# Kernel tuning notes

Hardware: AMD Instinct MI355X
Metric: run time of the kernel (lower is better)

The kernel has to match this reference:

```python
import jax, jax.numpy as jnp
import numpy as np
from jax import lax

E = 1024      # embed_dim
H = 16        # num_heads
HD = E // H   # head_dim = 64
GS = 2        # head_group_size
G = H // GS   # num head groups = 8
KQ = 3        # kq kernel q size
KK = 3        # kq kernel k size


def setup_inputs() -> dict:
    key = jax.random.key(0)
    ks = jax.random.split(key, 18)
    B, S = 2, 1024
    def rn(k, shape, scale=1.0):
        return jax.random.normal(k, shape, dtype=jnp.float32) * scale
    return {
        "Q": rn(ks[0], (B, S, E)),
        "K": rn(ks[1], (B, S, E)),
        "V": rn(ks[2], (B, S, E)),
        "Wq": rn(ks[3], (E, E), 0.02), "bq": rn(ks[4], (E,), 0.02),
        "Wk": rn(ks[5], (E, E), 0.02), "bk": rn(ks[6], (E,), 0.02),
        "Wv": rn(ks[7], (E, E), 0.02), "bv": rn(ks[8], (E,), 0.02),
        "Wo": rn(ks[9], (E, E), 0.02), "bo": rn(ks[10], (E,), 0.02),
        # depthwise key-query conv: [out=H, in/groups=1, KQ, KK]
        "kq_w": rn(ks[11], (H, 1, KQ, KK), 0.1),
        "kq_b": rn(ks[12], (H,), 0.02),
        # grouped 1x1 head-mix conv: weight [H, GS] (kernel dim squeezed), bias [H]
        "mix_w": rn(ks[13], (H, GS), 0.3),
        "mix_b": rn(ks[14], (H,), 0.02),
        # DynamicTanh params over head_dim (channels_last)
        "dyt_alpha": jnp.array([0.5], dtype=jnp.float32),
        "dyt_w": jnp.ones((HD,), dtype=jnp.float32),
        "dyt_b": jnp.zeros((HD,), dtype=jnp.float32),
        "depth_scale": jnp.ones((1,), dtype=jnp.float32),
    }


def reference(Q, K, V, Wq, bq, Wk, bk, Wv, bv, Wo, bo,
              kq_w, kq_b, mix_w, mix_b, dyt_alpha, dyt_w, dyt_b, depth_scale):
    B, S, _ = Q.shape
    scale = HD ** (-0.5)
    # projections -> [B, H, S, HD]
    q = (Q @ Wq + bq).reshape(B, S, H, HD).transpose(0, 2, 1, 3)
    k = (K @ Wk + bk).reshape(B, S, H, HD).transpose(0, 2, 1, 3)
    v = (V @ Wv + bv).reshape(B, S, H, HD).transpose(0, 2, 1, 3)

    # raw logits [B, H, Sq, Sk], multiplicative causal mask (zeros above diag)
    logits = jnp.einsum('bhqd,bhkd->bhqk', q, k) * scale
    causal = jnp.tril(jnp.ones((S, S), dtype=logits.dtype))
    logits = logits * causal

    # per-head (depthwise) key-query conv2d; torch pads q-dim by 2 both sides
    # then crops to first S rows (causal in q), k-dim padded symmetrically by 1
    conv = lax.conv_general_dilated(
        logits, kq_w, window_strides=(1, 1),
        padding=[(KQ - 1, KQ - 1), ((KK - 1) // 2, (KK - 1) // 2)],
        dimension_numbers=('NCHW', 'OIHW', 'NCHW'),
        feature_group_count=H)
    conv = conv + kq_b[None, :, None, None]
    conv = conv[:, :, :S, :]

    attn = jax.nn.softmax(conv, axis=-1)

    # grouped 1x1 head-mixing conv (within groups of GS heads) + bias
    attn_g = attn.reshape(B, G, GS, S, S)
    mw = mix_w.reshape(G, GS, GS)  # [group, out_in_group, in_in_group]
    mixed = jnp.einsum('goj,bgjqk->bgoqk', mw, attn_g).reshape(B, H, S, S)
    mixed = mixed + mix_b[None, :, None, None]

    out = jnp.einsum('bhqk,bhkd->bhqd', mixed, v)
    # DynamicTanh over head_dim (channels_last) + depth scale
    out = jnp.tanh(dyt_alpha * out) * dyt_w + dyt_b
    out = out * depth_scale
    out = out.transpose(0, 2, 1, 3).reshape(B, S, E)
    return out @ Wo + bo
```

## Files before the change

### kernel.cpp

```cpp
#include <hip/hip_runtime.h>
#include <cstdint>
#include <cstddef>

typedef __bf16 bf16;
typedef __bf16 bf16x8 __attribute__((ext_vector_type(8)));
typedef float f32x4 __attribute__((ext_vector_type(4)));

#define DEVI static __device__ __forceinline__

DEVI unsigned int cvt_pk_bf16(float lo, float hi) {
  unsigned int bl = __float_as_uint(lo);
  bl += 0x7fffu + ((bl >> 16) & 1u);
  unsigned int bh = __float_as_uint(hi);
  bh += 0x7fffu + ((bh >> 16) & 1u);
  return (bl >> 16) | (bh & 0xffff0000u);
}
DEVI float bf_lo(unsigned int u) { return __uint_as_float(u << 16); }
DEVI float bf_hi(unsigned int u) { return __uint_as_float(u & 0xffff0000u); }

DEVI void gload16(const bf16* g, bf16* l) {
  __builtin_amdgcn_global_load_lds(
      (const __attribute__((address_space(1))) unsigned int*)g,
      (__attribute__((address_space(3))) unsigned int*)l, 16, 0, 0);
}

__global__ __launch_bounds__(256) void prep_k(
    const float* __restrict__ Wq, const float* __restrict__ Wk,
    const float* __restrict__ Wv, const float* __restrict__ Wo,
    const float* __restrict__ Q, const float* __restrict__ K,
    const float* __restrict__ V, bf16* __restrict__ Wt,
    bf16* __restrict__ Ab)
{
  __shared__ bf16 Ts[64 * 72];
  const int bid = blockIdx.x, tid = threadIdx.x;
  if (bid < 1024) {
    const int z = bid >> 8;
    const float* W = (z == 0) ? Wq : (z == 1) ? Wk : (z == 2) ? Wv : Wo;
    bf16* out = Wt + ((size_t)z << 20);
    const int n0 = (bid & 15) * 64, k0 = ((bid >> 4) & 15) * 64;
    #pragma unroll
    for (int i = 0; i < 4; ++i) {
      int t = tid + i * 256;
      int kr = t >> 4, nc = t & 15;
      float4 v = *(const float4*)(W + (size_t)(k0 + kr) * 1024 + n0 + nc * 4);
      Ts[(nc * 4 + 0) * 72 + kr] = (bf16)v.x;
      Ts[(nc * 4 + 1) * 72 + kr] = (bf16)v.y;
      Ts[(nc * 4 + 2) * 72 + kr] = (bf16)v.z;
      Ts[(nc * 4 + 3) * 72 + kr] = (bf16)v.w;
    }
    __syncthreads();
    const int n = tid >> 2, kc = tid & 3;
    *(uint4*)(out + (size_t)(n0 + n) * 1024 + k0 + kc * 16) =
        *(const uint4*)(&Ts[n * 72 + kc * 16]);
    *(uint4*)(out + (size_t)(n0 + n) * 1024 + k0 + kc * 16 + 8) =
        *(const uint4*)(&Ts[n * 72 + kc * 16 + 8]);
  } else {
    const int t = bid - 1024;
    const int z = t >> 10, x = t & 1023;
    const float* A = (z == 0) ? Q : (z == 1) ? K : V;
    bf16* o = Ab + ((size_t)z << 21);
    const size_t idx = (size_t)x * 256 + tid;
    const float4 v0 = *(const float4*)(A + idx * 8);
    const float4 v1 = *(const float4*)(A + idx * 8 + 4);
    uint4 u;
    u.x = cvt_pk_bf16(v0.x, v0.y);
    u.y = cvt_pk_bf16(v0.z, v0.w);
    u.z = cvt_pk_bf16(v1.x, v1.y);
    u.w = cvt_pk_bf16(v1.z, v1.w);
    *(uint4*)(o + idx * 8) = u;
  }
}

__global__ __launch_bounds__(256) void proj_gemm_k(
    const bf16* __restrict__ Ab, const bf16* __restrict__ Wt,
    const float* __restrict__ bq, const float* __restrict__ bk,
    const float* __restrict__ bv, bf16* __restrict__ outbase,
    float* __restrict__ Tsum)
{
  const int z = blockIdx.z;
  const bf16* A  = Ab + ((size_t)z << 21);
  const bf16* Bt = Wt + ((size_t)z << 20);
  const float* bias = (z == 0) ? bq : (z == 1) ? bk : bv;
  bf16* outb = outbase + ((size_t)z << 21);

  __shared__ __align__(16) bf16 Asm[2][8192];
  __shared__ __align__(16) bf16 Bsm[2][4096];

  const int tid = threadIdx.x, lane = tid & 63, wid = tid >> 6;
  const int q4 = lane >> 4, n16 = lane & 15;
  const int wm = wid >> 1, wn = wid & 1;
  const int bid = blockIdx.x;
  const int m0 = (bid & 15) * 128, n0 = (bid >> 4) * 64;

  const int cbase = wid * 64 + lane;
  const bf16* gA[4];
  #pragma unroll
  for (int i = 0; i < 4; ++i) {
    int cc = cbase + i * 256;
    gA[i] = A + (size_t)(m0 + (cc >> 3)) * 1024 + (((cc & 7) ^ ((cc >> 3) & 7)) << 3);
  }
  const bf16* gB[2];
  #pragma unroll
  for (int i = 0; i < 2; ++i) {
    int cc = cbase + i * 256;
    gB[i] = Bt + (size_t)(n0 + (cc >> 3)) * 1024 + (((cc & 7) ^ ((cc >> 3) & 7)) << 3);
  }
  const int swl = n16 & 7;

  f32x4 acc[4][2] = {};

  #pragma unroll
  for (int i = 0; i < 4; ++i) gload16(gA[i], &Asm[0][i * 2048 + wid * 512]);
  #pragma unroll
  for (int i = 0; i < 2; ++i) gload16(gB[i], &Bsm[0][i * 2048 + wid * 512]);
  __syncthreads();

  int cur = 0;
  for (int t = 0; t < 16; ++t) {
    if (t < 15) {
      const int kc = (t + 1) * 64;
      #pragma unroll
      for (int i = 0; i < 4; ++i) gload16(gA[i] + kc, &Asm[cur ^ 1][i * 2048 + wid * 512]);
      #pragma unroll
      for (int i = 0; i < 2; ++i) gload16(gB[i] + kc, &Bsm[cur ^ 1][i * 2048 + wid * 512]);
    }
    const char* ab = (const char*)&Asm[cur][0];
    const char* bb = (const char*)&Bsm[cur][0];
    bf16x8 af[2][4], bfv[2][2];
    #pragma unroll
    for (int kk2 = 0; kk2 < 2; ++kk2) {
      #pragma unroll
      for (int rt = 0; rt < 4; ++rt)
        af[kk2][rt] = *(const bf16x8*)(ab + (wm * 64 + rt * 16 + n16) * 128 +
                                       (((kk2 * 4 + q4) ^ swl) << 4));
      #pragma unroll
      for (int ct = 0; ct < 2; ++ct)
        bfv[kk2][ct] = *(const bf16x8*)(bb + (wn * 32 + ct * 16 + n16) * 128 +
                                        (((kk2 * 4 + q4) ^ swl) << 4));
    }
    #pragma unroll
    for (int kk2 = 0; kk2 < 2; ++kk2)
      #pragma unroll
      for (int rt = 0; rt < 4; ++rt)
        #pragma unroll
        for (int ct = 0; ct < 2; ++ct)
          acc[rt][ct] = __builtin_amdgcn_mfma_f32_16x16x32_bf16(af[kk2][rt], bfv[kk2][ct], acc[rt][ct], 0, 0, 0);
    __syncthreads();
    cur ^= 1;
  }

  if (z < 2) {
    const int h = n0 >> 6;
    #pragma unroll
    for (int ct = 0; ct < 2; ++ct) {
      const int dl = wn * 32 + ct * 16 + n16;
      const float bvl = bias[n0 + dl];
      #pragma unroll
      for (int rt = 0; rt < 4; ++rt) {
        #pragma unroll
        for (int r = 0; r < 4; ++r) {
          int row = m0 + wm * 64 + rt * 16 + q4 * 4 + r;
          int b2 = row >> 10, s = row & 1023;
          outb[((size_t)((b2 * 16 + h) * 1024 + s) << 6) + dl] =
              (bf16)(acc[rt][ct][r] + bvl);
        }
      }
    }
  } else {
    const int b2 = m0 >> 10, kt0 = (m0 & 1023) >> 6, hh = n0 >> 6;
    bf16* vout = outb + ((size_t)(b2 * 16 + hh) << 16) + (size_t)(kt0 + wm) * 4096;
    float csum[2] = {0.f, 0.f};
    #pragma unroll
    for (int rt = 0; rt < 4; ++rt) {
      const int kk = rt >> 1;
      const int q4c = (rt & 1) * 2 + (q4 >> 1);
      const int jo = (q4 & 1) * 4;
      #pragma unroll
      for (int ct = 0; ct < 2; ++ct) {
        const int cl = wn * 32 + ct * 16 + n16;
        const float bvl = bias[n0 + cl];
        unsigned int p0 = cvt_pk_bf16(acc[rt][ct][0] + bvl, acc[rt][ct][1] + bvl);
        unsigned int p1 = cvt_pk_bf16(acc[rt][ct][2] + bvl, acc[rt][ct][3] + bvl);
        csum[ct] += bf_lo(p0) + bf_hi(p0) + bf_lo(p1) + bf_hi(p1);
        *(uint2*)(vout + kk * 2048 + (wn * 2 + ct) * 512 + (q4c * 16 + n16) * 8 + jo) =
            make_uint2(p0, p1);
      }
    }
    #pragma unroll
    for (int ct = 0; ct < 2; ++ct) {
      csum[ct] += __shfl_xor(csum[ct], 16);
      csum[ct] += __shfl_xor(csum[ct], 32);
    }
    if (lane < 16) {
      float* tsd = Tsum + ((size_t)(b2 * 16 + hh) * 16 + kt0 + wm) * 64 + wn * 32 + n16;
      tsd[0]  = csum[0];
      tsd[16] = csum[1];
    }
  }
}

__global__ __launch_bounds__(256) void out_gemm_k(
    const bf16* __restrict__ Ab, const bf16* __restrict__ Bt,
    const float* __restrict__ bias, float* __restrict__ outf)
{
  __shared__ __align__(16) bf16 Asm[2][4096];
  __shared__ __align__(16) bf16 Bsm[2][4096];
  const int tid = threadIdx.x, lane = tid & 63, wid = tid >> 6;
  const int q4 = lane >> 4, n16 = lane & 15;
  const int wm = wid >> 1, wn = wid & 1;
  const int bid = blockIdx.x;
  const int m0 = (bid & 31) * 64, n0 = (bid >> 5) * 64;
  const int cbase = wid * 64 + lane;
  const bf16* gA[2];
  const bf16* gB[2];
  #pragma unroll
  for (int i = 0; i < 2; ++i) {
    int cc = cbase + i * 256;
    gA[i] = Ab + (size_t)(m0 + (cc >> 3)) * 1024 + (((cc & 7) ^ ((cc >> 3) & 7)) << 3);
    gB[i] = Bt + (size_t)(n0 + (cc >> 3)) * 1024 + (((cc & 7) ^ ((cc >> 3) & 7)) << 3);
  }
  const int swl = n16 & 7;
  f32x4 acc[2][2] = {};

  #pragma unroll
  for (int i = 0; i < 2; ++i) {
    gload16(gA[i], &Asm[0][i * 2048 + wid * 512]);
    gload16(gB[i], &Bsm[0][i * 2048 + wid * 512]);
  }
  __syncthreads();

  int cur = 0;
  for (int t = 0; t < 16; ++t) {
    if (t < 15) {
      const int kc = (t + 1) * 64;
      #pragma unroll
      for (int i = 0; i < 2; ++i) {
        gload16(gA[i] + kc, &Asm[cur ^ 1][i * 2048 + wid * 512]);
        gload16(gB[i] + kc, &Bsm[cur ^ 1][i * 2048 + wid * 512]);
      }
    }
    const char* ab = (const char*)&Asm[cur][0];
    const char* bb = (const char*)&Bsm[cur][0];
    bf16x8 af[2][2], bfv[2][2];
    #pragma unroll
    for (int kk2 = 0; kk2 < 2; ++kk2) {
      #pragma unroll
      for (int rt = 0; rt < 2; ++rt)
        af[kk2][rt] = *(const bf16x8*)(ab + (wm * 32 + rt * 16 + n16) * 128 +
                                       (((kk2 * 4 + q4) ^ swl) << 4));
      #pragma unroll
      for (int ct = 0; ct < 2; ++ct)
        bfv[kk2][ct] = *(const bf16x8*)(bb + (wn * 32 + ct * 16 + n16) * 128 +
                                        (((kk2 * 4 + q4) ^ swl) << 4));
    }
    #pragma unroll
    for (int kk2 = 0; kk2 < 2; ++kk2)
      #pragma unroll
      for (int rt = 0; rt < 2; ++rt)
        #pragma unroll
        for (int ct = 0; ct < 2; ++ct)
          acc[rt][ct] = __builtin_amdgcn_mfma_f32_16x16x32_bf16(af[kk2][rt], bfv[kk2][ct], acc[rt][ct], 0, 0, 0);
    __syncthreads();
    cur ^= 1;
  }
  #pragma unroll
  for (int ct = 0; ct < 2; ++ct) {
    int col = n0 + wn * 32 + ct * 16 + n16;
    float bvl = bias[col];
    #pragma unroll
    for (int rt = 0; rt < 2; ++rt)
      #pragma unroll
      for (int r = 0; r < 4; ++r) {
        int row = m0 + wm * 32 + rt * 16 + q4 * 4 + r;
        outf[(size_t)row * 1024 + col] = acc[rt][ct][r] + bvl;
      }
  }
}

__global__ __launch_bounds__(320) void logits_conv_k(
    const bf16* __restrict__ qh, const bf16* __restrict__ kh,
    const float* __restrict__ kq_w, const float* __restrict__ kq_b,
    bf16* __restrict__ conv_out, float* __restrict__ tstats,
    const float* __restrict__ Tsum, float* __restrict__ Vtail)
{
  const int tt = blockIdx.x;
  const int h = blockIdx.y, b = blockIdx.z;
  if (tt == 151) {
    const int d = threadIdx.x;
    if (d < 64) {
      float* vt = Vtail + (size_t)(b * 16 + h) * 17 * 64;
      vt[16 * 64 + d] = 0.f;
      float c = 0.f;
      for (int kt = 15; kt >= 0; --kt) {
        c += Tsum[((size_t)(b * 16 + h) * 16 + kt) * 64 + d];
        vt[kt * 64 + d] = c;
      }
    }
    return;
  }
  int qt = 0, base = 0;
  while (qt < 15 && base + qt + 2 <= tt) { base += qt + 2; ++qt; }
  const int ct = tt - base;
  const int q0 = qt * 64, c0 = ct * 64;
  __shared__ __align__(16) char un[18432];
  bf16* Kst = (bf16*)un;
  float* Ls = (float*)un;
  const int tid = threadIdx.x;
  const int lane = tid & 63, wid = tid >> 6;
  const int q4 = lane >> 4, n16 = lane & 15;
  const bf16* qb = qh + ((size_t)(b * 16 + h) << 16);
  const bf16* kb = kh + ((size_t)(b * 16 + h) << 16);

  const int ar = min(max(q0 - 2 + wid * 16 + n16, 0), 1023);
  bf16x8 a0 = *(const bf16x8*)(qb + ar * 64 + q4 * 8);
  bf16x8 a1 = *(const bf16x8*)(qb + ar * 64 + 32 + q4 * 8);

  for (int t = tid; t < 640; t += 320) {
    int row = t >> 3, ch = t & 7;
    int br = min(max(c0 - 1 + row, 0), 1023);
    *(uint4*)(&Kst[row * 72 + ch * 8]) = *(const uint4*)(kb + br * 64 + ch * 8);
  }
  __syncthreads();

  f32x4 acc[5] = {};
  #pragma unroll
  for (int c5 = 0; c5 < 5; ++c5) {
    int brow = c5 * 16 + n16;
    bf16x8 b0 = *(const bf16x8*)(&Kst[brow * 72 + q4 * 8]);
    bf16x8 b1 = *(const bf16x8*)(&Kst[brow * 72 + 32 + q4 * 8]);
    acc[c5] = __builtin_amdgcn_mfma_f32_16x16x32_bf16(a0, b0, acc[c5], 0, 0, 0);
    acc[c5] = __builtin_amdgcn_mfma_f32_16x16x32_bf16(a1, b1, acc[c5], 0, 0, 0);
  }
  __syncthreads();

  #pragma unroll
  for (int c5 = 0; c5 < 5; ++c5) {
    #pragma unroll
    for (int r = 0; r < 4; ++r) {
      int Lrow = wid * 16 + q4 * 4 + r;
      int Lcol = c5 * 16 + n16;
      if (Lrow < 66 && Lcol < 66) {
        int rg = q0 - 2 + Lrow;
        int cg = c0 - 1 + Lcol;
        float v = (cg >= 0 && cg <= rg) ? acc[c5][r] * 0.125f : 0.f;
        Ls[Lrow * 68 + Lcol] = v;
      }
    }
  }
  __syncthreads();

  if (tid < 256) {
    float w9[9];
    #pragma unroll
    for (int i = 0; i < 9; ++i) w9[i] = kq_w[h * 9 + i];
    const float bb = kq_b[h];
    const size_t tplane = (size_t)(b * 16 + h) * 151 + base + ct;
    bf16* tb = conv_out + tplane * 4096;
    float2* st = (float2*)tstats + tplane * 64;

    const int r = tid >> 2, qr = tid & 3;
    float4 R0[5], R1[5], R2[5];
    const float* L0 = &Ls[r * 68 + qr * 16];
    #pragma unroll
    for (int i = 0; i < 5; ++i) {
      R0[i] = *(const float4*)(L0 + i * 4);
      R1[i] = *(const float4*)(L0 + 68 + i * 4);
      R2[i] = *(const float4*)(L0 + 136 + i * 4);
    }
    const float* f0 = (const float*)R0;
    const float* f1 = (const float*)R1;
    const float* f2 = (const float*)R2;
    float o[16];
    #pragma unroll
    for (int jj = 0; jj < 16; ++jj)
      o[jj] = bb + w9[0]*f0[jj] + w9[1]*f0[jj+1] + w9[2]*f0[jj+2]
                 + w9[3]*f1[jj] + w9[4]*f1[jj+1] + w9[5]*f1[jj+2]
                 + w9[6]*f2[jj] + w9[7]*f2[jj+1] + w9[8]*f2[jj+2];
    float mx = o[0];
    #pragma unroll
    for (int jj = 1; jj < 16; ++jj) mx = fmaxf(mx, o[jj]);
    mx = fmaxf(mx, __shfl_xor(mx, 1));
    mx = fmaxf(mx, __shfl_xor(mx, 2));
    unsigned int p[8];
    #pragma unroll
    for (int jj = 0; jj < 8; ++jj)
      p[jj] = cvt_pk_bf16(__expf(o[2*jj] - mx), __expf(o[2*jj+1] - mx));
    const int kk = qr >> 1, q4b = (qr & 1) * 2, sr = r >> 4, n16r = r & 15;
    *(uint4*)(tb + (sr * 2 + kk) * 512 + (q4b * 16 + n16r) * 8)       = *(const uint4*)&p[0];
    *(uint4*)(tb + (sr * 2 + kk) * 512 + ((q4b + 1) * 16 + n16r) * 8) = *(const uint4*)&p[4];
    float s = 0.f;
    #pragma unroll
    for (int jj = 0; jj < 8; ++jj) s += bf_lo(p[jj]) + bf_hi(p[jj]);
    s += __shfl_xor(s, 1);
    s += __shfl_xor(s, 2);
    if (qr == 0) st[r] = make_float2(mx, s);
  }
}

__global__ __launch_bounds__(256) void pv_k(
    const bf16* __restrict__ conv_out, const bf16* __restrict__ V2,
    const float* __restrict__ tstats, const float* __restrict__ Vtail,
    const float* __restrict__ mix_w, const float* __restrict__ mix_b,
    const float* __restrict__ kq_b,
    const float* __restrict__ dyt_alpha, const float* __restrict__ dyt_w,
    const float* __restrict__ dyt_b, const float* __restrict__ depth_scale,
    bf16* __restrict__ out_attn)
{
  const int qt16 = blockIdx.x, g = blockIdx.y, b = blockIdx.z;
  const int qt = qt16 >> 2;
  const int nkt = min(qt + 2, 16);
  const int Tc = 1024 - (nkt << 6);
  const int tid = threadIdx.x, lane = tid & 63, wid = tid >> 6;
  const int q4 = lane >> 4, n16 = lane & 15;
  const int oo = wid >> 1, kh = wid & 1;
  const int h0 = 2 * g, ho = h0 + oo;
  const int sr = qt16 & 3, strow = sr * 16;
  const size_t tbase = (size_t)(qt * (qt + 3) / 2);

  __shared__ float2 rsS[2][16];
  if (tid < 32) {
    const int hh = tid >> 4, rw = tid & 15;
    const float2* tsp = (const float2*)tstats +
        ((size_t)(b * 16 + h0 + hh) * 151 + tbase) * 64 + strow + rw;
    const float kb2 = kq_b[h0 + hh];
    float mx = (Tc > 0) ? kb2 : -3.0e38f;
    for (int kt = 0; kt < nkt; ++kt) mx = fmaxf(mx, tsp[(size_t)kt * 64].x);
    float s = (float)Tc * __expf(kb2 - mx);
    for (int kt = 0; kt < nkt; ++kt) {
      float2 v = tsp[(size_t)kt * 64];
      s += v.y * __expf(v.x - mx);
    }
    rsS[hh][rw] = make_float2(mx, 1.f / s);
  }
  __syncthreads();

  const float2 r0 = rsS[0][n16];
  const float2 r1 = rsS[1][n16];
  const float m0 = r0.x, m1 = r1.x;
  const float mwa = mix_w[ho * 2 + 0], mwb = mix_w[ho * 2 + 1];
  const float wa = mwa * r0.y, wb = mwb * r1.y;

  const bf16* pb0 = conv_out +
      ((size_t)(b * 16 + h0) * 151 + tbase) * 4096 + sr * 1024 + lane * 8;
  const bf16* pb1 = pb0 + (size_t)151 * 4096;
  const float2* ts0 = (const float2*)tstats +
      ((size_t)(b * 16 + h0) * 151 + tbase) * 64 + strow + n16;
  const float2* ts1 = ts0 + (size_t)151 * 64;
  const bf16* vb = V2 + ((size_t)(b * 16 + ho) << 16) + lane * 8;

  const int niter = (nkt - kh + 1) >> 1;
  float wk0[8], wk1[8];
  #pragma unroll
  for (int i = 0; i < 8; ++i) {
    int ktc = (i < niter) ? (kh + 2 * i) : 0;
    wk0[i] = wa * __expf(ts0[(size_t)ktc * 64].x - m0);
    wk1[i] = wb * __expf(ts1[(size_t)ktc * 64].x - m1);
  }

  f32x4 acc[4] = {};
  int ii = 0;
  for (int kt = kh; kt < nkt; kt += 2, ++ii) {
    uint4 u0[2], u1[2];
    #pragma unroll
    for (int kk = 0; kk < 2; ++kk) {
      u0[kk] = *(const uint4*)(pb0 + (size_t)kt * 4096 + kk * 512);
      u1[kk] = *(const uint4*)(pb1 + (size_t)kt * 4096 + kk * 512);
    }
    bf16x8 bv[2][4];
    #pragma unroll
    for (int kk = 0; kk < 2; ++kk)
      #pragma unroll
      for (int ctt = 0; ctt < 4; ++ctt)
        bv[kk][ctt] = *(const bf16x8*)(vb + (size_t)kt * 4096 + kk * 2048 + ctt * 512);
    const float w0 = wk0[ii], w1 = wk1[ii];
    #pragma unroll
    for (int kk = 0; kk < 2; ++kk) {
      bf16x8 af;
      const unsigned int* a0p = (const unsigned int*)&u0[kk];
      const unsigned int* a1p = (const unsigned int*)&u1[kk];
      #pragma unroll
      for (int i2 = 0; i2 < 4; ++i2) {
        float a0 = w0 * bf_lo(a0p[i2]) + w1 * bf_lo(a1p[i2]);
        float a1 = w0 * bf_hi(a0p[i2]) + w1 * bf_hi(a1p[i2]);
        ((unsigned int*)&af)[i2] = cvt_pk_bf16(a0, a1);
      }
      #pragma unroll
      for (int ctt = 0; ctt < 4; ++ctt)
        acc[ctt] = __builtin_amdgcn_mfma_f32_16x16x32_bf16(af, bv[kk][ctt], acc[ctt], 0, 0, 0);
    }
  }

  __shared__ float Pp[2][16][66];
  if (kh == 1) {
    #pragma unroll
    for (int ctt = 0; ctt < 4; ++ctt)
      #pragma unroll
      for (int r = 0; r < 4; ++r)
        Pp[oo][q4 * 4 + r][ctt * 16 + n16] = acc[ctt][r];
  }
  __syncthreads();
  if (kh == 1) return;
  #pragma unroll
  for (int ctt = 0; ctt < 4; ++ctt)
    #pragma unroll
    for (int r = 0; r < 4; ++r)
      acc[ctt][r] += Pp[oo][q4 * 4 + r][ctt * 16 + n16];

  const float kqb0 = kq_b[h0], kqb1 = kq_b[h0 + 1];
  float tw[4];
  #pragma unroll
  for (int r = 0; r < 4; ++r) {
    float2 s0 = rsS[0][q4 * 4 + r];
    float2 s1 = rsS[1][q4 * 4 + r];
    tw[r] = (Tc > 0) ? (mwa * s0.y * __expf(kqb0 - s0.x) +
                        mwb * s1.y * __expf(kqb1 - s1.x)) : 0.f;
  }
  const float mb = mix_b[ho];
  const float alpha = dyt_alpha[0], dsc = depth_scale[0];
  const float* vt = Vtail + (size_t)(b * 16 + ho) * 17 * 64;
  #pragma unroll
  for (int ctt = 0; ctt < 4; ++ctt) {
    int d = ctt * 16 + n16;
    float vtn = vt[(size_t)nkt * 64 + d];
    float vt0 = vt[d];
    float wgt = dyt_w[d], bds = dyt_b[d];
    #pragma unroll
    for (int r = 0; r < 4; ++r) {
      float v = acc[ctt][r] + tw[r] * vtn + mb * vt0;
      float e = __expf(2.f * alpha * v);
      float th = 1.f - 2.f / (e + 1.f);
      float y = (th * wgt + bds) * dsc;
      int qr = qt16 * 16 + q4 * 4 + r;
      out_attn[(((size_t)(b * 1024 + qr)) << 10) + ho * 64 + d] = (bf16)y;
    }
  }
}

extern "C" void kernel_launch(void* const* d_in, const int* in_sizes, int n_in,
                              void* d_out, int out_size, void* d_ws, size_t ws_size,
                              hipStream_t stream) {
  const float* Q    = (const float*)d_in[0];
  const float* Kx   = (const float*)d_in[1];
  const float* V    = (const float*)d_in[2];
  const float* Wq   = (const float*)d_in[3];
  const float* bq   = (const float*)d_in[4];
  const float* Wk   = (const float*)d_in[5];
  const float* bk   = (const float*)d_in[6];
  const float* Wv   = (const float*)d_in[7];
  const float* bv   = (const float*)d_in[8];
  const float* Wo   = (const float*)d_in[9];
  const float* bo   = (const float*)d_in[10];
  const float* kq_w = (const float*)d_in[11];
  const float* kq_b = (const float*)d_in[12];
  const float* mixw = (const float*)d_in[13];
  const float* mixb = (const float*)d_in[14];
  const float* dyta = (const float*)d_in[15];
  const float* dytw = (const float*)d_in[16];
  const float* dytb = (const float*)d_in[17];
  const float* dsc  = (const float*)d_in[18];

  char* ws = (char*)d_ws;
  bf16* qh     = (bf16*)(ws);
  float* tstat = (float*)(ws + (size_t)(12 << 20));
  float* Vtail = (float*)(ws + (size_t)(16 << 20));
  float* Tsum  = (float*)(ws + (size_t)(16 << 20) + (256 << 10));
  bf16* WtT    = (bf16*)(ws + (size_t)(17 << 20));
  bf16* oat    = (bf16*)(ws + (size_t)(17 << 20));
  bf16* conv   = (bf16*)(ws + (size_t)(25 << 20));
  bf16* Ab     = (bf16*)(ws + (size_t)(25 << 20));
  bf16* kh     = qh + ((size_t)1 << 21);
  bf16* V2     = qh + ((size_t)2 << 21);

  prep_k<<<dim3(4096), 256, 0, stream>>>(Wq, Wk, Wv, Wo, Q, Kx, V, WtT, Ab);
  proj_gemm_k<<<dim3(256, 1, 3), 256, 0, stream>>>(Ab, WtT, bq, bk, bv, qh, Tsum);
  logits_conv_k<<<dim3(152, 16, 2), 320, 0, stream>>>(qh, kh, kq_w, kq_b, conv, tstat,
                                                      Tsum, Vtail);
  pv_k<<<dim3(64, 8, 2), 256, 0, stream>>>(conv, V2, tstat, Vtail, mixw, mixb, kq_b,
                                           dyta, dytw, dytb, dsc, oat);
  out_gemm_k<<<dim3(512), 256, 0, stream>>>(oat, WtT + ((size_t)3 << 20), bo, (float*)d_out);
}
```

Measured before the change: 200.6 us.

## Deepen GEMM prefetch so two K-tiles are in flight, using explicit vmcnt waits

Both projection GEMM kernels now issue the loads for the first two K-tiles up front. Each iteration waits with a partial vmcnt so only the current tile has landed, then reads fragments into registers and barriers. It then issues the load for tile t+2 into the buffer just consumed before running the MFMAs. The aim is to keep more global-to-LDS traffic overlapped with compute and to drop the trailing __syncthreads. It relies on hand-counted vmcnt values and sched barriers, which could break if the compiler emits extra memory ops.

```diff
diff --git a/kernel.cpp b/kernel.cpp
--- a/kernel.cpp
+++ b/kernel.cpp
@@ -113,17 +113,18 @@
   for (int i = 0; i < 4; ++i) gload16(gA[i], &Asm[0][i * 2048 + wid * 512]);
   #pragma unroll
   for (int i = 0; i < 2; ++i) gload16(gB[i], &Bsm[0][i * 2048 + wid * 512]);
-  __syncthreads();
+  #pragma unroll
+  for (int i = 0; i < 4; ++i) gload16(gA[i] + 64, &Asm[1][i * 2048 + wid * 512]);
+  #pragma unroll
+  for (int i = 0; i < 2; ++i) gload16(gB[i] + 64, &Bsm[1][i * 2048 + wid * 512]);
 
   int cur = 0;
+  #pragma unroll 1
   for (int t = 0; t < 16; ++t) {
-    if (t < 15) {
-      const int kc = (t + 1) * 64;
-      #pragma unroll
-      for (int i = 0; i < 4; ++i) gload16(gA[i] + kc, &Asm[cur ^ 1][i * 2048 + wid * 512]);
-      #pragma unroll
-      for (int i = 0; i < 2; ++i) gload16(gB[i] + kc, &Bsm[cur ^ 1][i * 2048 + wid * 512]);
-    }
+    if (t < 15) { asm volatile("s_waitcnt vmcnt(6)" ::: "memory"); }
+    else        { asm volatile("s_waitcnt vmcnt(0)" ::: "memory"); }
+    __builtin_amdgcn_sched_barrier(0);
+    __builtin_amdgcn_s_barrier();
     const char* ab = (const char*)&Asm[cur][0];
     const char* bb = (const char*)&Bsm[cur][0];
     bf16x8 af[2][4], bfv[2][2];
@@ -137,6 +138,16 @@
       for (int ct = 0; ct < 2; ++ct)
         bfv[kk2][ct] = *(const bf16x8*)(bb + (wn * 32 + ct * 16 + n16) * 128 +
                                         (((kk2 * 4 + q4) ^ swl) << 4));
+    }
+    asm volatile("s_waitcnt lgkmcnt(0)" ::: "memory");
+    __builtin_amdgcn_sched_barrier(0);
+    __builtin_amdgcn_s_barrier();
+    if (t < 14) {
+      const int kc = (t + 2) * 64;
+      #pragma unroll
+      for (int i = 0; i < 4; ++i) gload16(gA[i] + kc, &Asm[cur][i * 2048 + wid * 512]);
+      #pragma unroll
+      for (int i = 0; i < 2; ++i) gload16(gB[i] + kc, &Bsm[cur][i * 2048 + wid * 512]);
     }
     #pragma unroll
     for (int kk2 = 0; kk2 < 2; ++kk2)
@@ -145,7 +156,6 @@
         #pragma unroll
         for (int ct = 0; ct < 2; ++ct)
           acc[rt][ct] = __builtin_amdgcn_mfma_f32_16x16x32_bf16(af[kk2][rt], bfv[kk2][ct], acc[rt][ct], 0, 0, 0);
-    __syncthreads();
     cur ^= 1;
   }
 
@@ -227,18 +237,19 @@
     gload16(gA[i], &Asm[0][i * 2048 + wid * 512]);
     gload16(gB[i], &Bsm[0][i * 2048 + wid * 512]);
   }
-  __syncthreads();
+  #pragma unroll
+  for (int i = 0; i < 2; ++i) {
+    gload16(gA[i] + 64, &Asm[1][i * 2048 + wid * 512]);
+    gload16(gB[i] + 64, &Bsm[1][i * 2048 + wid * 512]);
+  }
 
   int cur = 0;
+  #pragma unroll 1
   for (int t = 0; t < 16; ++t) {
-    if (t < 15) {
-      const int kc = (t + 1) * 64;
-      #pragma unroll
-      for (int i = 0; i < 2; ++i) {
-        gload16(gA[i] + kc, &Asm[cur ^ 1][i * 2048 + wid * 512]);
-        gload16(gB[i] + kc, &Bsm[cur ^ 1][i * 2048 + wid * 512]);
-      }
-    }
+    if (t < 15) { asm volatile("s_waitcnt vmcnt(4)" ::: "memory"); }
+    else        { asm volatile("s_waitcnt vmcnt(0)" ::: "memory"); }
+    __builtin_amdgcn_sched_barrier(0);
+    __builtin_amdgcn_s_barrier();
     const char* ab = (const char*)&Asm[cur][0];
     const char* bb = (const char*)&Bsm[cur][0];
     bf16x8 af[2][2], bfv[2][2];
@@ -252,6 +263,17 @@
       for (int ct = 0; ct < 2; ++ct)
         bfv[kk2][ct] = *(const bf16x8*)(bb + (wn * 32 + ct * 16 + n16) * 128 +
                                         (((kk2 * 4 + q4) ^ swl) << 4));
+    }
+    asm volatile("s_waitcnt lgkmcnt(0)" ::: "memory");
+    __builtin_amdgcn_sched_barrier(0);
+    __builtin_amdgcn_s_barrier();
+    if (t < 14) {
+      const int kc = (t + 2) * 64;
+      #pragma unroll
+      for (int i = 0; i < 2; ++i) {
+        gload16(gA[i] + kc, &Asm[cur][i * 2048 + wid * 512]);
+        gload16(gB[i] + kc, &Bsm[cur][i * 2048 + wid * 512]);
+      }
     }
     #pragma unroll
     for (int kk2 = 0; kk2 < 2; ++kk2)
@@ -260,7 +282,6 @@
         #pragma unroll
         for (int ct = 0; ct < 2; ++ct)
           acc[rt][ct] = __builtin_amdgcn_mfma_f32_16x16x32_bf16(af[kk2][rt], bfv[kk2][ct], acc[rt][ct], 0, 0, 0);
-    __syncthreads();
     cur ^= 1;
   }
   #pragma unroll
```

After: 196.4 us. -2.1%, faster.
